# Kernel optimization log

Hardware: AMD Instinct MI355X
Metric: run time of the kernel (lower is better)

## Reference

```python
import math
import numpy as np
import jax
import jax.numpy as jnp

RANK = 8
KITER = 2
EPS = 1e-5


def frft_time(z, alpha):
    # z: complex64 [B, T, C]; fractional Fourier transform along axis 1
    # via Bluestein-style chirp multiplication + FFT convolution.
    T = z.shape[1]
    a = (float(alpha) + math.pi) % (2.0 * math.pi) - math.pi
    if abs(a) < 1e-6:
        return z
    if abs(abs(a) - math.pi) < 1e-6:
        ph = np.complex64(np.exp(1j * math.copysign(math.pi / 2, a)))
        return ph * jnp.flip(z, axis=1)
    sa = math.sin(a)
    s = math.copysign(1.0 / max(1e-7, abs(sa)), sa)
    c = math.cos(a) / max(1e-7, sa)
    t = np.linspace(-1.0, 1.0, T)
    dt = 2.0 / (T - 1)
    tail = (1,) * (z.ndim - 2)
    pre = jnp.asarray(np.exp(1j * np.pi * (c + s) * t ** 2).astype(np.complex64)).reshape(1, T, *tail)
    g = z * pre
    m = np.arange(-(T - 1), T)
    L = 1 << (2 * T - 2).bit_length()  # next pow2 >= 2T-1
    h_pad = np.zeros(L, np.complex64)
    h_pad[m % L] = np.exp(-1j * np.pi * s * (m * dt) ** 2).astype(np.complex64)
    H = jnp.asarray(np.fft.fft(h_pad).astype(np.complex64)).reshape(1, L, *tail)
    pad = [(0, 0), (0, L - T)] + [(0, 0)] * (z.ndim - 2)
    G = jnp.fft.fft(jnp.pad(g, pad), axis=1)
    conv = jnp.fft.ifft(G * H, axis=1)[:, T - 1:T - 1 + T]
    pref = np.complex64(np.sqrt(np.complex64(1.0 - 1j * c)))
    return pref * pre * conv * np.float32(dt)


def _orthonorm(V):
    # batched reduced QR with deterministic column signs (sign of diag(R))
    Q, R = jnp.linalg.qr(V)
    d = jnp.diagonal(R, axis1=-2, axis2=-1)
    return Q * jnp.sign(d + EPS)[:, None, :]


def _forward(x, Win_shift, Wout_shift, b_shift, W_out, ln_gamma, ln_beta):
    B, T, D = x.shape
    anchor = jnp.zeros((B, D), x.dtype).at[:, 0].set(1.0)
    xc = x - anchor[:, None, :]
    # LowRankShift: S(x) = W_out_shift @ gelu(W_in_shift @ x) + b
    s = jax.nn.gelu(x @ Win_shift.T, approximate=False) @ Wout_shift.T + b_shift
    xprime = xc + s
    xpc = xprime.astype(jnp.complex64)
    alphas = np.linspace(0.15, 2.99, RANK)
    # per-alpha FrFT-domain energy weights
    weights = []
    for alpha in alphas:
        X_a = frft_time(xpc, alpha)
        E_a = jnp.mean(jnp.abs(X_a) ** 2, axis=2)  # [B,T]
        w_a = jnp.sqrt(E_a + 1e-6)  # pow p=0.5
        w_a = w_a / (jnp.mean(w_a, axis=1, keepdims=True) + 1e-6)
        weights.append((float(alpha), w_a))

    def Komega(Y):  # Y: real [B,T,r]
        Yc = Y.astype(jnp.complex64)
        acc = 0.0
        for alpha, w in weights:
            Ya = frft_time(Yc, alpha)
            acc = acc + frft_time(w[..., None].astype(jnp.complex64) * Ya, -alpha)
        return (acc / len(weights)).real

    # subspace iteration with identity init
    E0 = jnp.zeros((B, D, RANK), x.dtype).at[:, :RANK, :].set(jnp.eye(RANK, dtype=x.dtype))
    V = _orthonorm(E0)
    for _ in range(KITER):
        Y = Komega(xprime @ V)  # [B,T,r]
        Z = jnp.einsum('btd,btr->bdr', xprime, Y) / float(T)
        V = _orthonorm(Z + EPS * V)
    # sign-align columns to anchor
    sgn = jnp.sign(jnp.sum(V * anchor[:, :, None], axis=1) + 1e-12)
    V = V * sgn[:, None, :]
    traces = xprime @ V  # [B,T,r]
    scales = jnp.sqrt(jnp.sum(traces ** 2, axis=1, keepdims=True) + EPS)
    traces_n = traces / scales
    # shrink_lambda == 0 -> soft_shrink identity; SpiralMix(rank=1) has no pairs -> identity
    traces_final = traces_n * scales
    x_tilde = jnp.einsum('btr,bdr->btd', traces_final, V)
    x_hat = x_tilde - s + anchor[:, None, :]
    y = x + x_hat @ W_out.T  # dropout eval mode
    mu = jnp.mean(y, axis=-1, keepdims=True)
    var = jnp.mean((y - mu) ** 2, axis=-1, keepdims=True)
    return (y - mu) / jnp.sqrt(var + 1e-5) * ln_gamma + ln_beta


def setup_inputs():
    key = jax.random.key(0)
    k = jax.random.split(key, 5)
    B, T, D, SR = 4, 2048, 256, 128
    return {
        'x': jax.random.normal(k[0], (B, T, D), jnp.float32),
        'Win_shift': jax.random.normal(k[1], (SR, D), jnp.float32) / np.float32(np.sqrt(D)),
        'Wout_shift': jax.random.normal(k[2], (D, SR), jnp.float32) / np.float32(np.sqrt(SR)),
        'b_shift': jax.random.normal(k[3], (D,), jnp.float32) * 0.01,
        'W_out': jax.random.normal(k[4], (D, D), jnp.float32) / np.float32(np.sqrt(D)),
        'ln_gamma': jnp.ones((D,), jnp.float32),
        'ln_beta': jnp.zeros((D,), jnp.float32),
    }


def reference(x, Win_shift, Wout_shift, b_shift, W_out, ln_gamma, ln_beta):
    return _forward(x, Win_shift, Wout_shift, b_shift, W_out, ln_gamma, ln_beta)
```

## Files before the change

### kernel.cpp

```cpp
#include <hip/hip_runtime.h>
#include <math.h>

#define Bb 4
#define Tt 2048
#define Dd 256
#define SRr 128
#define Rr 8
#define NA 8
#define NV 16
#define Lf 4096
#define EPSf 1e-5f
#define PI_D 3.14159265358979323846

#define OFF_TW4R  0
#define OFF_TW4I  (OFF_TW4R + 4096)
#define OFF_PRER  (OFF_TW4I + 4096)
#define OFF_PREI  (OFF_PRER + NV*Tt)
#define OFF_POSR  (OFF_PREI + NV*Tt)
#define OFF_POSI  (OFF_POSR + NV*Tt)
#define OFF_PM2   (OFF_POSI + NV*Tt)
#define OFF_H     (OFF_PM2 + NA*Tt)
#define OFF_WINT  (OFF_H + NV*Lf*2)
#define OFF_WOUTT (OFF_WINT + Dd*SRr)
#define OFF_WOT   (OFF_WOUTT + SRr*Dd)
#define OFF_WTAB  (OFF_WOT + Dd*Dd)
#define OFF_ESUM  (OFF_WTAB + NA*Bb*Tt)
#define OFF_V     (OFF_ESUM + NA*Bb*Tt)
#define OFF_M     (OFF_V + Bb*Dd*Rr)
#define OFF_YT    (OFF_M + Bb*Dd*Rr)
#define OFF_YAC8  (OFF_YT + Bb*Rr*Tt)
#define OFF_S     (OFF_YAC8 + NA*Bb*Rr*Tt)
#define OFF_XPT   (OFF_S + Bb*Tt*Dd)

__device__ __forceinline__ float block_reduce_sum(float v, float* red, int tid){
  #pragma unroll
  for (int o = 32; o > 0; o >>= 1) v += __shfl_xor(v, o, 64);
  __syncthreads();
  if ((tid & 63) == 0) red[tid >> 6] = v;
  __syncthreads();
  return red[0] + red[1] + red[2] + red[3];
}

__device__ void variant_params(int v, double& s_, double& c_){
  double step = (2.99 - 0.15) / 7.0;
  int idx = v & 7;
  double alpha = (idx == 7) ? 2.99 : (0.15 + (double)idx * step);
  if (v >= 8) alpha = -alpha;
  double a = fmod(alpha + PI_D, 2.0 * PI_D);
  if (a < 0.0) a += 2.0 * PI_D;
  a -= PI_D;
  double sa = sin(a);
  s_ = ((sa >= 0.0) ? 1.0 : -1.0) / fmax(1e-7, fabs(sa));
  c_ = cos(a) / fmax(1e-7, sa);
}

struct cpx { float r, i; };
__device__ __forceinline__ cpx cmul(cpx a, cpx b){ return {a.r*b.r - a.i*b.i, a.r*b.i + a.i*b.r}; }
__device__ __forceinline__ cpx cmulj(cpx a, cpx b){ return {a.r*b.r + a.i*b.i, a.i*b.r - a.r*b.i}; }

__device__ __forceinline__ void fft4(cpx& a, cpx& b, cpx& c, cpx& d, float sgn){
  cpx t0{a.r+c.r, a.i+c.i}, t1{a.r-c.r, a.i-c.i};
  cpx t2{b.r+d.r, b.i+d.i}, t3{b.r-d.r, b.i-d.i};
  a = {t0.r+t2.r, t0.i+t2.i};
  c = {t0.r-t2.r, t0.i-t2.i};
  b = {t1.r - sgn*t3.i, t1.i + sgn*t3.r};
  d = {t1.r + sgn*t3.i, t1.i - sgn*t3.r};
}

template<int ZP>
__device__ __forceinline__ void fft16(cpx x[16], float sgn){
  const float WC[10] = {1.f, 0.92387953251128674f, 0.70710678118654752f, 0.38268343236508977f,
                        0.f, -0.38268343236508977f, -0.70710678118654752f, -0.92387953251128674f,
                        -1.f, -0.92387953251128674f};
  const float WS[10] = {0.f, 0.38268343236508977f, 0.70710678118654752f, 0.92387953251128674f,
                        1.f, 0.92387953251128674f, 0.70710678118654752f, 0.38268343236508977f,
                        0.f, -0.38268343236508977f};
  if (ZP){
    #pragma unroll
    for (int j0 = 0; j0 < 4; ++j0){
      cpx a = x[j0], b = x[j0+4];
      x[j0]    = {a.r + b.r,       a.i + b.i};
      x[j0+4]  = {a.r - sgn*b.i,   a.i + sgn*b.r};
      x[j0+8]  = {a.r - b.r,       a.i - b.i};
      x[j0+12] = {a.r + sgn*b.i,   a.i - sgn*b.r};
    }
  } else {
    #pragma unroll
    for (int j0 = 0; j0 < 4; ++j0)
      fft4(x[j0], x[j0+4], x[j0+8], x[j0+12], sgn);
  }
  #pragma unroll
  for (int j0 = 1; j0 < 4; ++j0){
    #pragma unroll
    for (int p0 = 1; p0 < 4; ++p0){
      int m = j0*p0;
      cpx w{WC[m], sgn*WS[m]};
      x[j0 + 4*p0] = cmul(x[j0 + 4*p0], w);
    }
  }
  #pragma unroll
  for (int p0 = 0; p0 < 4; ++p0)
    fft4(x[4*p0+0], x[4*p0+1], x[4*p0+2], x[4*p0+3], sgn);
  cpx t;
  t=x[1];  x[1]=x[4];   x[4]=t;
  t=x[2];  x[2]=x[8];   x[8]=t;
  t=x[3];  x[3]=x[12];  x[12]=t;
  t=x[6];  x[6]=x[9];   x[9]=t;
  t=x[7];  x[7]=x[13];  x[13]=t;
  t=x[11]; x[11]=x[14]; x[14]=t;
}

template<int ZP>
__device__ __forceinline__ void fft4096c(cpx x[16], float2* sh,
                                         const cpx twA[16], const cpx twB[16],
                                         int tid, float sgn){
  int hi = tid >> 4, lo = tid & 15;
  fft16<ZP>(x, sgn);
  #pragma unroll
  for (int p = 1; p < 16; ++p) x[p] = (sgn < 0.f) ? cmul(x[p], twA[p]) : cmulj(x[p], twA[p]);
  __syncthreads();
  #pragma unroll
  for (int p = 0; p < 16; ++p){ sh[p*272 + 17*hi + lo] = make_float2(x[p].r, x[p].i); }
  __syncthreads();
  #pragma unroll
  for (int u = 0; u < 16; ++u){ float2 v = sh[hi*272 + 17*u + lo]; x[u] = {v.x, v.y}; }
  fft16<0>(x, sgn);
  #pragma unroll
  for (int q = 1; q < 16; ++q) x[q] = (sgn < 0.f) ? cmul(x[q], twB[q]) : cmulj(x[q], twB[q]);
  __syncthreads();
  #pragma unroll
  for (int q = 0; q < 16; ++q){ sh[hi*272 + 17*q + lo] = make_float2(x[q].r, x[q].i); }
  __syncthreads();
  #pragma unroll
  for (int v = 0; v < 16; ++v){ float2 t = sh[hi*272 + 17*lo + v]; x[v] = {t.x, t.y}; }
  fft16<0>(x, sgn);
}

__global__ __launch_bounds__(256) void k_setup(const float* Win, const float* Wout,
                                               const float* Wo, float* ws){
  __shared__ float2 sh[16*272];
  int blk = blockIdx.x, tid = threadIdx.x;
  int id = blk*256 + tid;
  { int d = id & (Dd-1); int k = id >> 8; ws[OFF_WOT + id] = Wo[d*Dd + k]; }
  if (id < Dd*SRr){
    int c = id & (SRr-1); int k = id >> 7;
    ws[OFF_WINT + id] = Win[c*Dd + k];
    int d2 = id & (Dd-1); int k2 = id >> 8;
    ws[OFF_WOUTT + id] = Wout[d2*SRr + k2];
  }
  if (id < 4096){
    double ang = -2.0 * PI_D * (double)id / (double)Lf;
    ws[OFF_TW4R + id] = (float)cos(ang);
    ws[OFF_TW4I + id] = (float)sin(ang);
  }
  if (blk >= NV) return;
  int v = blk;
  double s_, c_;
  variant_params(v, s_, c_);
  double dt = 2.0 / (double)(Tt - 1);
  {
    double cf = (double)(float)c_;
    double rmag = sqrt(1.0 + cf * cf);
    double pr = sqrt((rmag + 1.0) * 0.5);
    double pim = ((cf >= 0.0) ? -1.0 : 1.0) * sqrt(fmax(0.0, (rmag - 1.0) * 0.5));
    double cps = PI_D * (c_ + s_);
    double sc = dt / (double)Lf;
    for (int k = tid; k < Tt; k += 256){
      double t = (k == Tt - 1) ? 1.0 : ((double)k * dt - 1.0);
      double th = cps * (t * t);
      double cr = cos(th), ci = sin(th);
      ws[OFF_PRER + v*Tt + k] = (float)cr;
      ws[OFF_PREI + v*Tt + k] = (float)ci;
      float por = (float)((pr*cr - pim*ci) * sc);
      float poi = (float)((pr*ci + pim*cr) * sc);
      ws[OFF_POSR + v*Tt + k] = por;
      ws[OFF_POSI + v*Tt + k] = poi;
      if (v < NA) ws[OFF_PM2 + v*Tt + k] = por*por + poi*poi;
    }
  }
  int hi = tid >> 4, lo = tid & 15;
  int base = hi + 16*lo;
  cpx twA[16], twB[16];
  #pragma unroll
  for (int p = 0; p < 16; ++p){
    double aA = -2.0 * PI_D * (double)((tid * p) & 4095) / (double)Lf;
    double aB = -2.0 * PI_D * (double)((16 * lo * p) & 4095) / (double)Lf;
    twA[p] = {(float)cos(aA), (float)sin(aA)};
    twB[p] = {(float)cos(aB), (float)sin(aB)};
  }
  double ns = -(PI_D * s_);
  cpx x[16];
  #pragma unroll
  for (int j = 0; j < 16; ++j){
    int n = j*256 + tid;
    if (n == 2048){ x[j] = {0.f, 0.f}; continue; }
    int m = (n <= 2047) ? n : (n - 4096);
    double md = (double)m * dt;
    double th = ns * (md * md);
    x[j] = {(float)cos(th), (float)sin(th)};
  }
  fft4096c<0>(x, sh, twA, twB, tid, -1.f);
  #pragma unroll
  for (int r = 0; r < 16; ++r){
    int k = base + 256*r;
    ws[OFF_H + (v*Lf + k)*2 + 0] = x[r].r;
    ws[OFF_H + (v*Lf + k)*2 + 1] = x[r].i;
  }
}

__global__ __launch_bounds__(256) void k_shift(const float* x, const float* bsh, float* ws){
  __shared__ float xs[16][Dd];
  __shared__ float us[16][SRr];
  int tid = threadIdx.x;
  int g0 = blockIdx.x * 16;
  int b = g0 >> 11, t0 = g0 & (Tt - 1);
  #pragma unroll
  for (int row = 0; row < 16; ++row)
    xs[row][tid] = x[(g0 + row)*Dd + tid];
  __syncthreads();
  int col = tid & 127, rowgrp = tid >> 7;
  {
    float acc[8];
    #pragma unroll
    for (int rr = 0; rr < 8; ++rr) acc[rr] = 0.f;
    const float* WT = ws + OFF_WINT;
    for (int k = 0; k < Dd; ++k){
      float w = WT[k*SRr + col];
      #pragma unroll
      for (int rr = 0; rr < 8; ++rr)
        acc[rr] = fmaf(xs[rowgrp*8 + rr][k], w, acc[rr]);
    }
    #pragma unroll
    for (int rr = 0; rr < 8; ++rr){
      float a = acc[rr];
      us[rowgrp*8 + rr][col] = 0.5f * a * (1.0f + erff(a * 0.70710678118654752f));
    }
  }
  __syncthreads();
  float sacc[16];
  float bv = bsh[tid];
  #pragma unroll
  for (int row = 0; row < 16; ++row) sacc[row] = bv;
  const float* WT2 = ws + OFF_WOUTT;
  for (int k = 0; k < SRr; ++k){
    float w = WT2[k*Dd + tid];
    #pragma unroll
    for (int row = 0; row < 16; ++row)
      sacc[row] = fmaf(us[row][k], w, sacc[row]);
  }
  float xp[16];
  #pragma unroll
  for (int row = 0; row < 16; ++row){
    float xv = xs[row][tid];
    float anc = (tid == 0) ? 1.0f : 0.0f;
    ws[OFF_S + (g0 + row)*Dd + tid] = sacc[row];
    xp[row] = xv - anc + sacc[row];
  }
  float* xpt = ws + OFF_XPT + ((size_t)(b*Dd + tid))*Tt + t0;
  #pragma unroll
  for (int q = 0; q < 4; ++q)
    *reinterpret_cast<float4*>(xpt + 4*q) = make_float4(xp[4*q], xp[4*q+1], xp[4*q+2], xp[4*q+3]);
}

__global__ __launch_bounds__(256) void k_weights(float* ws){
  __shared__ float2 sh[16*272];
  int tid = threadIdx.x;
  int chunk = blockIdx.x, b = blockIdx.y, z = blockIdx.z;
  int hi = tid >> 4, lo = tid & 15;
  int base = hi + 16*lo;
  const float* tw4r = ws + OFF_TW4R; const float* tw4i = ws + OFF_TW4I;
  cpx twA[16], twB[16];
  #pragma unroll
  for (int p = 0; p < 16; ++p){
    int iA = tid * p;      twA[p] = {tw4r[iA], tw4i[iA]};
    int iB = 16 * lo * p;  twB[p] = {tw4r[iB], tw4i[iB]};
  }
  const float* prer = ws + OFF_PRER + z*Tt;
  const float* prei = ws + OFF_PREI + z*Tt;
  const float* pm2  = ws + OFF_PM2  + z*Tt;
  const float* Hv   = ws + OFF_H    + z*Lf*2;
  float e[16];
  #pragma unroll
  for (int r = 0; r < 16; ++r) e[r] = 0.f;
  for (int cc = 0; cc < 8; ++cc){
    int c = chunk*8 + cc;
    const float* xcol = ws + OFF_XPT + ((size_t)(b*Dd + c))*Tt;
    cpx x[16];
    #pragma unroll
    for (int j = 0; j < 8; ++j){
      int t = j*256 + tid;
      float xv = xcol[t];
      x[j] = {xv * prer[t], xv * prei[t]};
    }
    #pragma unroll
    for (int j = 8; j < 16; ++j) x[j] = {0.f, 0.f};
    fft4096c<1>(x, sh, twA, twB, tid, -1.f);
    #pragma unroll
    for (int r = 0; r < 16; ++r){
      int k = base + 256*r;
      cpx h{Hv[2*k], Hv[2*k+1]};
      x[r] = cmul(x[r], h);
    }
    __syncthreads();
    #pragma unroll
    for (int r = 0; r < 16; ++r){ sh[r*272 + 17*lo + hi] = make_float2(x[r].r, x[r].i); }
    __syncthreads();
    #pragma unroll
    for (int j = 0; j < 16; ++j){ float2 v = sh[j*272 + 17*hi + lo]; x[j] = {v.x, v.y}; }
    fft4096c<0>(x, sh, twA, twB, tid, +1.f);
    #pragma unroll
    for (int r = 0; r < 16; ++r){
      int k = base + 256*r;
      if (k >= 2047 && k < 4095){
        int t = k - 2047;
        e[r] += pm2[t] * (x[r].r*x[r].r + x[r].i*x[r].i);
      }
    }
  }
  float* Ez = ws + OFF_ESUM + (z*Bb + b)*Tt;
  #pragma unroll
  for (int r = 0; r < 16; ++r){
    int k = base + 256*r;
    if (k >= 2047 && k < 4095) atomicAdd(&Ez[k - 2047], e[r]);
  }
}

__global__ void k_wnorm(float* ws){
  __shared__ float red[4];
  int b = blockIdx.x, z = blockIdx.y, tid = threadIdx.x;
  const float* Ez = ws + OFF_ESUM + (z*Bb + b)*Tt;
  float* wz = ws + OFF_WTAB + (z*Bb + b)*Tt;
  float wr[8]; float psum = 0.f;
  #pragma unroll
  for (int k = 0; k < 8; ++k){
    float Ea = Ez[tid + k*256] * (1.0f / (float)Dd);
    wr[k] = sqrtf(Ea + 1e-6f);
    psum += wr[k];
  }
  float tot = block_reduce_sum(psum, red, tid);
  float inv = 1.0f / (tot / (float)Tt + 1e-6f);
  #pragma unroll
  for (int k = 0; k < 8; ++k) wz[tid + k*256] = wr[k] * inv;
}

__global__ void k_traces(float* ws){
  __shared__ float Vl[Dd*Rr];
  int tile = blockIdx.x, b = blockIdx.y, tid = threadIdx.x;
  for (int i = tid; i < Dd*Rr; i += 256) Vl[i] = ws[OFF_V + b*Dd*Rr + i];
  __syncthreads();
  int t = tile*256 + tid;
  float acc[Rr];
  #pragma unroll
  for (int r = 0; r < Rr; ++r) acc[r] = 0.f;
  const float* xp = ws + OFF_XPT + ((size_t)(b*Dd))*Tt + t;
  for (int d = 0; d < Dd; ++d){
    float xv = xp[(size_t)d*Tt];
    #pragma unroll
    for (int r = 0; r < Rr; ++r) acc[r] = fmaf(xv, Vl[d*Rr + r], acc[r]);
  }
  #pragma unroll
  for (int r = 0; r < Rr; ++r) ws[OFF_YT + (b*Rr + r)*Tt + t] = acc[r];
}

__global__ __launch_bounds__(256) void k_komega(float* ws, int useXPT){
  __shared__ float2 sh[16*272];
  int tid = threadIdx.x;
  int rr = blockIdx.x, b = blockIdx.y, z = blockIdx.z;
  int hi = tid >> 4, lo = tid & 15;
  int base = hi + 16*lo;
  int v1 = z, v2 = z + NA;
  const float* tw4r = ws + OFF_TW4R; const float* tw4i = ws + OFF_TW4I;
  cpx twA[16], twB[16];
  #pragma unroll
  for (int p = 0; p < 16; ++p){
    int iA = tid * p;      twA[p] = {tw4r[iA], tw4i[iA]};
    int iB = 16 * lo * p;  twB[p] = {tw4r[iB], tw4i[iB]};
  }
  const float* prer1 = ws + OFF_PRER + v1*Tt; const float* prei1 = ws + OFF_PREI + v1*Tt;
  const float* posr1 = ws + OFF_POSR + v1*Tt; const float* posi1 = ws + OFF_POSI + v1*Tt;
  const float* prer2 = ws + OFF_PRER + v2*Tt; const float* prei2 = ws + OFF_PREI + v2*Tt;
  const float* posr2 = ws + OFF_POSR + v2*Tt; const float* posi2 = ws + OFF_POSI + v2*Tt;
  const float* H1 = ws + OFF_H + v1*Lf*2;
  const float* H2 = ws + OFF_H + v2*Lf*2;
  const float* wz = ws + OFF_WTAB + (z*Bb + b)*Tt;
  const float* ycol = useXPT ? (ws + OFF_XPT + ((size_t)(b*Dd + rr))*Tt)
                             : (ws + OFF_YT + ((size_t)(b*Rr + rr))*Tt);
  float* yac = ws + OFF_YAC8 + ((size_t)((z*Bb + b)*Rr + rr))*Tt;
  cpx x[16];
  #pragma unroll
  for (int j = 0; j < 8; ++j){
    int t = j*256 + tid;
    float yv = ycol[t];
    x[j] = {yv * prer1[t], yv * prei1[t]};
  }
  #pragma unroll
  for (int j = 8; j < 16; ++j) x[j] = {0.f, 0.f};
  fft4096c<1>(x, sh, twA, twB, tid, -1.f);
  #pragma unroll
  for (int r = 0; r < 16; ++r){ int k = base + 256*r; cpx h{H1[2*k], H1[2*k+1]}; x[r] = cmul(x[r], h); }
  __syncthreads();
  #pragma unroll
  for (int r = 0; r < 16; ++r){ sh[r*272 + 17*lo + hi] = make_float2(x[r].r, x[r].i); }
  __syncthreads();
  #pragma unroll
  for (int j = 0; j < 16; ++j){ float2 v = sh[j*272 + 17*hi + lo]; x[j] = {v.x, v.y}; }
  fft4096c<0>(x, sh, twA, twB, tid, +1.f);
  __syncthreads();
  #pragma unroll
  for (int r = 0; r < 16; ++r){
    int k = base + 256*r;
    if (k >= 2047 && k < 4095){
      int t = k - 2047;
      float cr = x[r].r, ci = x[r].i;
      float wv = wz[t];
      float yar = (posr1[t]*cr - posi1[t]*ci) * wv;
      float yai = (posr1[t]*ci + posi1[t]*cr) * wv;
      float gr = yar*prer2[t] - yai*prei2[t];
      float gi = yar*prei2[t] + yai*prer2[t];
      int a = (t >> 8)*272 + 17*((t >> 4) & 15) + (t & 15);
      sh[a] = make_float2(gr, gi);
    }
  }
  __syncthreads();
  #pragma unroll
  for (int j = 0; j < 8; ++j){ float2 v = sh[j*272 + 17*hi + lo]; x[j] = {v.x, v.y}; }
  #pragma unroll
  for (int j = 8; j < 16; ++j) x[j] = {0.f, 0.f};
  fft4096c<1>(x, sh, twA, twB, tid, -1.f);
  #pragma unroll
  for (int r = 0; r < 16; ++r){ int k = base + 256*r; cpx h{H2[2*k], H2[2*k+1]}; x[r] = cmul(x[r], h); }
  __syncthreads();
  #pragma unroll
  for (int r = 0; r < 16; ++r){ sh[r*272 + 17*lo + hi] = make_float2(x[r].r, x[r].i); }
  __syncthreads();
  #pragma unroll
  for (int j = 0; j < 16; ++j){ float2 v = sh[j*272 + 17*hi + lo]; x[j] = {v.x, v.y}; }
  fft4096c<0>(x, sh, twA, twB, tid, +1.f);
  #pragma unroll
  for (int r = 0; r < 16; ++r){
    int k = base + 256*r;
    if (k >= 2047 && k < 4095){
      int t = k - 2047;
      yac[t] = posr2[t]*x[r].r - posi2[t]*x[r].i;
    }
  }
}

__global__ void k_ysum(float* ws){
  int i = (blockIdx.x*256 + threadIdx.x) * 4;
  float4 acc = make_float4(0.f, 0.f, 0.f, 0.f);
  #pragma unroll
  for (int z = 0; z < NA; ++z){
    float4 v = *reinterpret_cast<const float4*>(ws + OFF_YAC8 + (size_t)z*Bb*Rr*Tt + i);
    acc.x += v.x; acc.y += v.y; acc.z += v.z; acc.w += v.w;
  }
  *reinterpret_cast<float4*>(ws + OFF_YT + i) = acc;
}

__global__ void k_zm(float* ws, int useIdent){
  __shared__ float red[4];
  int d = blockIdx.x, b = blockIdx.y, tid = threadIdx.x;
  const float* xcol = ws + OFF_XPT + ((size_t)(b*Dd + d))*Tt;
  for (int r = 0; r < Rr; ++r){
    const float* ycol = ws + OFF_YT + (b*Rr + r)*Tt;
    float p = 0.f;
    for (int t = tid; t < Tt; t += 256) p = fmaf(xcol[t], ycol[t], p);
    float tot = block_reduce_sum(p, red, tid);
    if (tid == 0){
      float zval = tot / (float)(Tt * NA);
      float vprev = useIdent ? ((d == r) ? 1.f : 0.f) : ws[OFF_V + (b*Dd + d)*Rr + r];
      ws[OFF_M + (b*Dd + d)*Rr + r] = zval + EPSf * vprev;
    }
  }
}

__global__ void k_mgs(float* ws){
  __shared__ float q[Rr][Dd];
  __shared__ float red[4];
  int b = blockIdx.x, tid = threadIdx.x;
  float m[Rr];
  #pragma unroll
  for (int r = 0; r < Rr; ++r) m[r] = ws[OFF_M + (b*Dd + tid)*Rr + r];
  for (int r = 0; r < Rr; ++r){
    float v = m[r];
    for (int j = 0; j < r; ++j){
      float dotv = block_reduce_sum(q[j][tid] * v, red, tid);
      v = fmaf(-dotv, q[j][tid], v);
    }
    float n2 = block_reduce_sum(v * v, red, tid);
    q[r][tid] = v / sqrtf(n2);
    __syncthreads();
  }
  #pragma unroll
  for (int r = 0; r < Rr; ++r) ws[OFF_V + (b*Dd + tid)*Rr + r] = q[r][tid];
}

__global__ __launch_bounds__(256) void k_out(const float* x, const float* g, const float* be,
                                             float* ws, float* out){
  __shared__ float hs[16][Dd + 1];
  __shared__ float ytl[16][Rr];
  __shared__ float mv_mu[16], mv_rs[16];
  int tid = threadIdx.x;
  int g0 = blockIdx.x * 16;
  int b = g0 >> 11, t0 = g0 & (Tt - 1);
  if (tid < 128){
    int row = tid >> 3, r = tid & 7;
    ytl[row][r] = ws[OFF_YT + (b*Rr + r)*Tt + t0 + row];
  }
  float vr[Rr];
  {
    const float4* Vb = reinterpret_cast<const float4*>(ws + OFF_V + (b*Dd + tid)*Rr);
    float4 v0 = Vb[0], v1 = Vb[1];
    vr[0]=v0.x; vr[1]=v0.y; vr[2]=v0.z; vr[3]=v0.w;
    vr[4]=v1.x; vr[5]=v1.y; vr[6]=v1.z; vr[7]=v1.w;
  }
  __syncthreads();
  #pragma unroll
  for (int row = 0; row < 16; ++row){
    float acc = 0.f;
    #pragma unroll
    for (int r = 0; r < Rr; ++r) acc = fmaf(ytl[row][r], vr[r], acc);
    acc -= ws[OFF_S + (g0 + row)*Dd + tid];
    if (tid == 0) acc += 1.0f;
    hs[row][tid] = acc;
  }
  __syncthreads();
  float acc[16];
  #pragma unroll
  for (int row = 0; row < 16; ++row) acc[row] = x[(g0 + row)*Dd + tid];
  const float* WT = ws + OFF_WOT;
  for (int k = 0; k < Dd; ++k){
    float w = WT[k*Dd + tid];
    #pragma unroll
    for (int row = 0; row < 16; ++row)
      acc[row] = fmaf(hs[row][k], w, acc[row]);
  }
  __syncthreads();
  #pragma unroll
  for (int row = 0; row < 16; ++row) hs[row][tid] = acc[row];
  __syncthreads();
  {
    int row = tid >> 4, j = tid & 15;
    float yv[16]; float sum = 0.f;
    #pragma unroll
    for (int mth = 0; mth < 16; ++mth){ yv[mth] = hs[row][j + 16*mth]; sum += yv[mth]; }
    #pragma unroll
    for (int o = 8; o > 0; o >>= 1) sum += __shfl_xor(sum, o, 16);
    float mu = sum * (1.0f / (float)Dd);
    float ssq = 0.f;
    #pragma unroll
    for (int mth = 0; mth < 16; ++mth){ float d = yv[mth] - mu; ssq = fmaf(d, d, ssq); }
    #pragma unroll
    for (int o = 8; o > 0; o >>= 1) ssq += __shfl_xor(ssq, o, 16);
    if (j == 0){ mv_mu[row] = mu; mv_rs[row] = rsqrtf(ssq * (1.0f / (float)Dd) + 1e-5f); }
  }
  __syncthreads();
  float gg = g[tid], bb = be[tid];
  #pragma unroll
  for (int row = 0; row < 16; ++row)
    out[(g0 + row)*Dd + tid] = (acc[row] - mv_mu[row]) * mv_rs[row] * gg + bb;
}

extern "C" void kernel_launch(void* const* d_in, const int* in_sizes, int n_in,
                              void* d_out, int out_size, void* d_ws, size_t ws_size,
                              hipStream_t stream){
  (void)in_sizes; (void)n_in; (void)out_size; (void)ws_size;
  const float* x    = (const float*)d_in[0];
  const float* Win  = (const float*)d_in[1];
  const float* Wout = (const float*)d_in[2];
  const float* bsh  = (const float*)d_in[3];
  const float* Wo   = (const float*)d_in[4];
  const float* g    = (const float*)d_in[5];
  const float* be   = (const float*)d_in[6];
  float* ws  = (float*)d_ws;
  float* out = (float*)d_out;

  hipLaunchKernelGGL(k_setup, dim3(256), dim3(256), 0, stream, Win, Wout, Wo, ws);
  hipLaunchKernelGGL(k_shift, dim3(Bb*Tt/16), dim3(256), 0, stream, x, bsh, ws);
  hipMemsetAsync(ws + OFF_ESUM, 0, (size_t)NA*Bb*Tt*sizeof(float), stream);
  hipLaunchKernelGGL(k_weights, dim3(Dd/8, Bb, NA), dim3(256), 0, stream, ws);
  hipLaunchKernelGGL(k_wnorm, dim3(Bb, NA), dim3(256), 0, stream, ws);
  hipLaunchKernelGGL(k_komega, dim3(Rr, Bb, NA), dim3(256), 0, stream, ws, 1);
  hipLaunchKernelGGL(k_ysum, dim3(64), dim3(256), 0, stream, ws);
  hipLaunchKernelGGL(k_zm, dim3(Dd, Bb), dim3(256), 0, stream, ws, 1);
  hipLaunchKernelGGL(k_mgs, dim3(Bb), dim3(256), 0, stream, ws);
  hipLaunchKernelGGL(k_traces, dim3(Tt/256, Bb), dim3(256), 0, stream, ws);
  hipLaunchKernelGGL(k_komega, dim3(Rr, Bb, NA), dim3(256), 0, stream, ws, 0);
  hipLaunchKernelGGL(k_ysum, dim3(64), dim3(256), 0, stream, ws);
  hipLaunchKernelGGL(k_zm, dim3(Dd, Bb), dim3(256), 0, stream, ws, 0);
  hipLaunchKernelGGL(k_mgs, dim3(Bb), dim3(256), 0, stream, ws);
  hipLaunchKernelGGL(k_traces, dim3(Tt/256, Bb), dim3(256), 0, stream, ws);
  hipLaunchKernelGGL(k_out, dim3(Bb*Tt/16), dim3(256), 0, stream, x, g, be, ws, out);
}
```

Measured before the change: 455.4 us.

## Reuse first-pass FrFT results from weights kernel and make MGS single-wave

The weights kernel already computes the forward FrFT of the first Rr columns of x'. It now stores those post-chirped outputs in a new workspace region (chunk 0 only). In its first invocation, k_komega reads that stored data instead of redoing an FFT, H multiply and inverse FFT, removing about half of that kernel's work. The epilogue loops also start at r=7 to skip rows that cannot be in the output range, k_zm keeps its x column in registers, and k_mgs becomes a single 64-lane wave using shuffle reductions with no block syncs. The cost is extra workspace and global writes in the weights kernel, plus a larger workspace requirement.

```diff
diff --git a/kernel.cpp b/kernel.cpp
--- a/kernel.cpp
+++ b/kernel.cpp
@@ -31,6 +31,7 @@
 #define OFF_YAC8  (OFF_YT + Bb*Rr*Tt)
 #define OFF_S     (OFF_YAC8 + NA*Bb*Rr*Tt)
 #define OFF_XPT   (OFF_S + Bb*Tt*Dd)
+#define OFF_F     (OFF_XPT + Bb*Tt*Dd)
 
 __device__ __forceinline__ float block_reduce_sum(float v, float* red, int tid){
   #pragma unroll
@@ -39,6 +40,12 @@
   if ((tid & 63) == 0) red[tid >> 6] = v;
   __syncthreads();
   return red[0] + red[1] + red[2] + red[3];
+}
+
+__device__ __forceinline__ float wave_sum(float v){
+  #pragma unroll
+  for (int o = 32; o > 0; o >>= 1) v += __shfl_xor(v, o, 64);
+  return v;
 }
 
 __device__ void variant_params(int v, double& s_, double& c_){
@@ -279,9 +286,9 @@
   const float* prei = ws + OFF_PREI + z*Tt;
   const float* pm2  = ws + OFF_PM2  + z*Tt;
   const float* Hv   = ws + OFF_H    + z*Lf*2;
-  float e[16];
-  #pragma unroll
-  for (int r = 0; r < 16; ++r) e[r] = 0.f;
+  float e[9];
+  #pragma unroll
+  for (int r = 0; r < 9; ++r) e[r] = 0.f;
   for (int cc = 0; cc < 8; ++cc){
     int c = chunk*8 + cc;
     const float* xcol = ws + OFF_XPT + ((size_t)(b*Dd + c))*Tt;
@@ -309,19 +316,34 @@
     for (int j = 0; j < 16; ++j){ float2 v = sh[j*272 + 17*hi + lo]; x[j] = {v.x, v.y}; }
     fft4096c<0>(x, sh, twA, twB, tid, +1.f);
     #pragma unroll
-    for (int r = 0; r < 16; ++r){
+    for (int r = 7; r < 16; ++r){
       int k = base + 256*r;
       if (k >= 2047 && k < 4095){
         int t = k - 2047;
-        e[r] += pm2[t] * (x[r].r*x[r].r + x[r].i*x[r].i);
+        e[r-7] += pm2[t] * (x[r].r*x[r].r + x[r].i*x[r].i);
       }
     }
+    if (chunk == 0){
+      const float* posr = ws + OFF_POSR + z*Tt;
+      const float* posi = ws + OFF_POSI + z*Tt;
+      float* Fp = ws + OFF_F + ((size_t)((z*Bb + b)*Rr + cc))*Tt*2;
+      #pragma unroll
+      for (int r = 7; r < 16; ++r){
+        int k = base + 256*r;
+        if (k >= 2047 && k < 4095){
+          int t = k - 2047;
+          float por = posr[t], poi = posi[t];
+          Fp[2*t]   = por*x[r].r - poi*x[r].i;
+          Fp[2*t+1] = por*x[r].i + poi*x[r].r;
+        }
+      }
+    }
   }
   float* Ez = ws + OFF_ESUM + (z*Bb + b)*Tt;
   #pragma unroll
-  for (int r = 0; r < 16; ++r){
+  for (int r = 7; r < 16; ++r){
     int k = base + 256*r;
-    if (k >= 2047 && k < 4095) atomicAdd(&Ez[k - 2047], e[r]);
+    if (k >= 2047 && k < 4095) atomicAdd(&Ez[k - 2047], e[r-7]);
   }
 }
 
@@ -362,7 +384,7 @@
   for (int r = 0; r < Rr; ++r) ws[OFF_YT + (b*Rr + r)*Tt + t] = acc[r];
 }
 
-__global__ __launch_bounds__(256) void k_komega(float* ws, int useXPT){
+__global__ __launch_bounds__(256) void k_komega(float* ws, int mode){
   __shared__ float2 sh[16*272];
   int tid = threadIdx.x;
   int rr = blockIdx.x, b = blockIdx.y, z = blockIdx.z;
@@ -376,56 +398,69 @@
     int iA = tid * p;      twA[p] = {tw4r[iA], tw4i[iA]};
     int iB = 16 * lo * p;  twB[p] = {tw4r[iB], tw4i[iB]};
   }
-  const float* prer1 = ws + OFF_PRER + v1*Tt; const float* prei1 = ws + OFF_PREI + v1*Tt;
-  const float* posr1 = ws + OFF_POSR + v1*Tt; const float* posi1 = ws + OFF_POSI + v1*Tt;
   const float* prer2 = ws + OFF_PRER + v2*Tt; const float* prei2 = ws + OFF_PREI + v2*Tt;
   const float* posr2 = ws + OFF_POSR + v2*Tt; const float* posi2 = ws + OFF_POSI + v2*Tt;
-  const float* H1 = ws + OFF_H + v1*Lf*2;
   const float* H2 = ws + OFF_H + v2*Lf*2;
   const float* wz = ws + OFF_WTAB + (z*Bb + b)*Tt;
-  const float* ycol = useXPT ? (ws + OFF_XPT + ((size_t)(b*Dd + rr))*Tt)
-                             : (ws + OFF_YT + ((size_t)(b*Rr + rr))*Tt);
   float* yac = ws + OFF_YAC8 + ((size_t)((z*Bb + b)*Rr + rr))*Tt;
   cpx x[16];
-  #pragma unroll
-  for (int j = 0; j < 8; ++j){
-    int t = j*256 + tid;
-    float yv = ycol[t];
-    x[j] = {yv * prer1[t], yv * prei1[t]};
-  }
-  #pragma unroll
-  for (int j = 8; j < 16; ++j) x[j] = {0.f, 0.f};
-  fft4096c<1>(x, sh, twA, twB, tid, -1.f);
-  #pragma unroll
-  for (int r = 0; r < 16; ++r){ int k = base + 256*r; cpx h{H1[2*k], H1[2*k+1]}; x[r] = cmul(x[r], h); }
-  __syncthreads();
-  #pragma unroll
-  for (int r = 0; r < 16; ++r){ sh[r*272 + 17*lo + hi] = make_float2(x[r].r, x[r].i); }
-  __syncthreads();
-  #pragma unroll
-  for (int j = 0; j < 16; ++j){ float2 v = sh[j*272 + 17*hi + lo]; x[j] = {v.x, v.y}; }
-  fft4096c<0>(x, sh, twA, twB, tid, +1.f);
-  __syncthreads();
-  #pragma unroll
-  for (int r = 0; r < 16; ++r){
-    int k = base + 256*r;
-    if (k >= 2047 && k < 4095){
-      int t = k - 2047;
-      float cr = x[r].r, ci = x[r].i;
+  if (mode){
+    const float* Fp = ws + OFF_F + ((size_t)((z*Bb + b)*Rr + rr))*Tt*2;
+    #pragma unroll
+    for (int j = 0; j < 8; ++j){
+      int t = j*256 + tid;
+      float fr = Fp[2*t], fi = Fp[2*t+1];
       float wv = wz[t];
-      float yar = (posr1[t]*cr - posi1[t]*ci) * wv;
-      float yai = (posr1[t]*ci + posi1[t]*cr) * wv;
-      float gr = yar*prer2[t] - yai*prei2[t];
-      float gi = yar*prei2[t] + yai*prer2[t];
-      int a = (t >> 8)*272 + 17*((t >> 4) & 15) + (t & 15);
-      sh[a] = make_float2(gr, gi);
-    }
-  }
-  __syncthreads();
-  #pragma unroll
-  for (int j = 0; j < 8; ++j){ float2 v = sh[j*272 + 17*hi + lo]; x[j] = {v.x, v.y}; }
-  #pragma unroll
-  for (int j = 8; j < 16; ++j) x[j] = {0.f, 0.f};
+      float yar = fr*wv, yai = fi*wv;
+      x[j] = {yar*prer2[t] - yai*prei2[t], yar*prei2[t] + yai*prer2[t]};
+    }
+    #pragma unroll
+    for (int j = 8; j < 16; ++j) x[j] = {0.f, 0.f};
+  } else {
+    const float* prer1 = ws + OFF_PRER + v1*Tt; const float* prei1 = ws + OFF_PREI + v1*Tt;
+    const float* posr1 = ws + OFF_POSR + v1*Tt; const float* posi1 = ws + OFF_POSI + v1*Tt;
+    const float* H1 = ws + OFF_H + v1*Lf*2;
+    const float* ycol = ws + OFF_YT + ((size_t)(b*Rr + rr))*Tt;
+    #pragma unroll
+    for (int j = 0; j < 8; ++j){
+      int t = j*256 + tid;
+      float yv = ycol[t];
+      x[j] = {yv * prer1[t], yv * prei1[t]};
+    }
+    #pragma unroll
+    for (int j = 8; j < 16; ++j) x[j] = {0.f, 0.f};
+    fft4096c<1>(x, sh, twA, twB, tid, -1.f);
+    #pragma unroll
+    for (int r = 0; r < 16; ++r){ int k = base + 256*r; cpx h{H1[2*k], H1[2*k+1]}; x[r] = cmul(x[r], h); }
+    __syncthreads();
+    #pragma unroll
+    for (int r = 0; r < 16; ++r){ sh[r*272 + 17*lo + hi] = make_float2(x[r].r, x[r].i); }
+    __syncthreads();
+    #pragma unroll
+    for (int j = 0; j < 16; ++j){ float2 v = sh[j*272 + 17*hi + lo]; x[j] = {v.x, v.y}; }
+    fft4096c<0>(x, sh, twA, twB, tid, +1.f);
+    __syncthreads();
+    #pragma unroll
+    for (int r = 0; r < 16; ++r){
+      int k = base + 256*r;
+      if (k >= 2047 && k < 4095){
+        int t = k - 2047;
+        float cr = x[r].r, ci = x[r].i;
+        float wv = wz[t];
+        float yar = (posr1[t]*cr - posi1[t]*ci) * wv;
+        float yai = (posr1[t]*ci + posi1[t]*cr) * wv;
+        float gr = yar*prer2[t] - yai*prei2[t];
+        float gi = yar*prei2[t] + yai*prer2[t];
+        int a = (t >> 8)*272 + 17*((t >> 4) & 15) + (t & 15);
+        sh[a] = make_float2(gr, gi);
+      }
+    }
+    __syncthreads();
+    #pragma unroll
+    for (int j = 0; j < 8; ++j){ float2 v = sh[j*272 + 17*hi + lo]; x[j] = {v.x, v.y}; }
+    #pragma unroll
+    for (int j = 8; j < 16; ++j) x[j] = {0.f, 0.f};
+  }
   fft4096c<1>(x, sh, twA, twB, tid, -1.f);
   #pragma unroll
   for (int r = 0; r < 16; ++r){ int k = base + 256*r; cpx h{H2[2*k], H2[2*k+1]}; x[r] = cmul(x[r], h); }
@@ -461,10 +496,14 @@
   __shared__ float red[4];
   int d = blockIdx.x, b = blockIdx.y, tid = threadIdx.x;
   const float* xcol = ws + OFF_XPT + ((size_t)(b*Dd + d))*Tt;
+  float xv[8];
+  #pragma unroll
+  for (int j = 0; j < 8; ++j) xv[j] = xcol[tid + 256*j];
   for (int r = 0; r < Rr; ++r){
     const float* ycol = ws + OFF_YT + (b*Rr + r)*Tt;
     float p = 0.f;
-    for (int t = tid; t < Tt; t += 256) p = fmaf(xcol[t], ycol[t], p);
+    #pragma unroll
+    for (int j = 0; j < 8; ++j) p = fmaf(xv[j], ycol[tid + 256*j], p);
     float tot = block_reduce_sum(p, red, tid);
     if (tid == 0){
       float zval = tot / (float)(Tt * NA);
@@ -474,25 +513,40 @@
   }
 }
 
-__global__ void k_mgs(float* ws){
-  __shared__ float q[Rr][Dd];
-  __shared__ float red[4];
-  int b = blockIdx.x, tid = threadIdx.x;
-  float m[Rr];
-  #pragma unroll
-  for (int r = 0; r < Rr; ++r) m[r] = ws[OFF_M + (b*Dd + tid)*Rr + r];
+__global__ __launch_bounds__(64) void k_mgs(float* ws){
+  int b = blockIdx.x, lane = threadIdx.x;
+  float m[Rr][4];
+  #pragma unroll
   for (int r = 0; r < Rr; ++r){
-    float v = m[r];
+    #pragma unroll
+    for (int q = 0; q < 4; ++q)
+      m[r][q] = ws[OFF_M + (size_t)(b*Dd + lane + 64*q)*Rr + r];
+  }
+  #pragma unroll
+  for (int r = 0; r < Rr; ++r){
+    #pragma unroll
     for (int j = 0; j < r; ++j){
-      float dotv = block_reduce_sum(q[j][tid] * v, red, tid);
-      v = fmaf(-dotv, q[j][tid], v);
-    }
-    float n2 = block_reduce_sum(v * v, red, tid);
-    q[r][tid] = v / sqrtf(n2);
-    __syncthreads();
-  }
-  #pragma unroll
-  for (int r = 0; r < Rr; ++r) ws[OFF_V + (b*Dd + tid)*Rr + r] = q[r][tid];
+      float p = 0.f;
+      #pragma unroll
+      for (int q = 0; q < 4; ++q) p = fmaf(m[j][q], m[r][q], p);
+      float dotv = wave_sum(p);
+      #pragma unroll
+      for (int q = 0; q < 4; ++q) m[r][q] = fmaf(-dotv, m[j][q], m[r][q]);
+    }
+    float p = 0.f;
+    #pragma unroll
+    for (int q = 0; q < 4; ++q) p = fmaf(m[r][q], m[r][q], p);
+    float n2 = wave_sum(p);
+    float s = sqrtf(n2);
+    #pragma unroll
+    for (int q = 0; q < 4; ++q) m[r][q] = m[r][q] / s;
+  }
+  #pragma unroll
+  for (int r = 0; r < Rr; ++r){
+    #pragma unroll
+    for (int q = 0; q < 4; ++q)
+      ws[OFF_V + (size_t)(b*Dd + lane + 64*q)*Rr + r] = m[r][q];
+  }
 }
 
 __global__ __launch_bounds__(256) void k_out(const float* x, const float* g, const float* be,
@@ -583,12 +637,12 @@
   hipLaunchKernelGGL(k_komega, dim3(Rr, Bb, NA), dim3(256), 0, stream, ws, 1);
   hipLaunchKernelGGL(k_ysum, dim3(64), dim3(256), 0, stream, ws);
   hipLaunchKernelGGL(k_zm, dim3(Dd, Bb), dim3(256), 0, stream, ws, 1);
-  hipLaunchKernelGGL(k_mgs, dim3(Bb), dim3(256), 0, stream, ws);
+  hipLaunchKernelGGL(k_mgs, dim3(Bb), dim3(64), 0, stream, ws);
   hipLaunchKernelGGL(k_traces, dim3(Tt/256, Bb), dim3(256), 0, stream, ws);
   hipLaunchKernelGGL(k_komega, dim3(Rr, Bb, NA), dim3(256), 0, stream, ws, 0);
   hipLaunchKernelGGL(k_ysum, dim3(64), dim3(256), 0, stream, ws);
   hipLaunchKernelGGL(k_zm, dim3(Dd, Bb), dim3(256), 0, stream, ws, 0);
-  hipLaunchKernelGGL(k_mgs, dim3(Bb), dim3(256), 0, stream, ws);
+  hipLaunchKernelGGL(k_mgs, dim3(Bb), dim3(64), 0, stream, ws);
   hipLaunchKernelGGL(k_traces, dim3(Tt/256, Bb), dim3(256), 0, stream, ws);
   hipLaunchKernelGGL(k_out, dim3(Bb*Tt/16), dim3(256), 0, stream, x, g, be, ws, out);
 }
```

Result: slower. 580.5 us (+27.5%).
